# Kernel tuning notes

Hardware: AMD Instinct MI355X
Metric: run time of the kernel (lower is better)

The kernel has to match this reference:

```python
import jax, jax.numpy as jnp
import numpy as np

B, T, C = 4, 2048, 1024


def setup_inputs() -> dict:
    key = jax.random.key(0)
    ks = jax.random.split(key, 5)
    s = 1.0 / np.sqrt(C)
    return {
        "X": jax.random.normal(ks[0], (B, T, C), dtype=jnp.float32),
        "Wq": jax.random.normal(ks[1], (C, C), dtype=jnp.float32) * s,
        "Wk": jax.random.normal(ks[2], (C, C), dtype=jnp.float32) * s,
        "Wv": jax.random.normal(ks[3], (C, C), dtype=jnp.float32) * s,
        "Wo": jax.random.normal(ks[4], (C, C), dtype=jnp.float32) * s,
    }


def reference(X, Wq, Wk, Wv, Wo):
    Bx, Tx, Cx = X.shape
    Q = X @ Wq  # [B,T,C]
    K = X @ Wk
    V = X @ Wv
    scores = jnp.einsum('btc,bsc->bts', Q, K) / jnp.sqrt(jnp.asarray(Cx, X.dtype))
    # causal mask: position t attends to s <= t
    causal = jnp.tril(jnp.ones((Tx, Tx), dtype=bool))
    scores = jnp.where(causal, scores, jnp.asarray(-jnp.inf, scores.dtype))
    weights = jax.nn.softmax(scores, axis=-1)
    out = jnp.einsum('bts,bsc->btc', weights, V)
    return out @ Wo
```

## Files before the change

### kernel.cpp

```cpp
#include <hip/hip_runtime.h>
#include <hip/hip_bf16.h>
#include <cmath>


typedef __attribute__((ext_vector_type(8))) __bf16 bf16x8;
typedef __attribute__((ext_vector_type(8))) short short8;
typedef __attribute__((ext_vector_type(4))) float f32x4;

__device__ __forceinline__ unsigned short f2bf(float f) {
  union { float f; unsigned u; } v; v.f = f;
  unsigned u = v.u;
  u += ((u >> 16) & 1u) + 0x7fffu;
  return (unsigned short)(u >> 16);
}
__device__ __forceinline__ float bf2f(unsigned short h) {
  union { unsigned u; float f; } v; v.u = ((unsigned)h) << 16;
  return v.f;
}

#define GLDS(gp, sp)                                                           \
  __builtin_amdgcn_global_load_lds(                                            \
      (const __attribute__((address_space(1))) void*)(gp),                     \
      (__attribute__((address_space(3))) void*)(sp), 16, 0, 0)

__global__ void cast_kernel(const float* __restrict__ src,
                            unsigned short* __restrict__ dst, int n) {
  int i = (blockIdx.x * blockDim.x + threadIdx.x) * 4;
  if (i >= n) return;
  float4 f = *(const float4*)(src + i);
  ushort4 o = make_ushort4(f2bf(f.x), f2bf(f.y), f2bf(f.z), f2bf(f.w));
  *(ushort4*)(dst + i) = o;
}

__global__ void transpose_cast(const float* __restrict__ src,
                               unsigned short* __restrict__ dst,
                               int rows, int cols) {
  __shared__ float tile[32][33];
  int bx = blockIdx.x * 32;
  int by = blockIdx.y * 32;
  int tx = threadIdx.x;
  int ty = threadIdx.y;
#pragma unroll
  for (int i = 0; i < 32; i += 8)
    tile[ty + i][tx] = src[(size_t)(by + ty + i) * cols + bx + tx];
  __syncthreads();
#pragma unroll
  for (int i = 0; i < 32; i += 8)
    dst[(size_t)(bx + ty + i) * rows + by + tx] = f2bf(tile[tx][ty + i]);
}

template <typename OutT>
__global__ __launch_bounds__(256, 2)
void gemm_bt(const unsigned short* __restrict__ A, int lda, long long sA,
             const unsigned short* __restrict__ B, int ldb, long long sB,
             OutT* __restrict__ Cp, int ldc, long long sC,
             int K, float alpha, int tri, int kcap) {
  A  += (long long)blockIdx.z * sA;
  B  += (long long)blockIdx.z * sB;
  Cp += (long long)blockIdx.z * sC;

  int by, bx;
  if (tri) {
    const int idx = blockIdx.x;
    by = (int)((sqrtf(8.f * idx + 1.f) - 1.f) * 0.5f);
    while (by * (by + 1) / 2 > idx) --by;
    while ((by + 1) * (by + 2) / 2 <= idx) ++by;
    bx = idx - by * (by + 1) / 2;
  } else {
    by = blockIdx.y;
    bx = blockIdx.x;
  }
  const int m0 = by * 128;
  const int n0 = bx * 128;
  const int Keff = kcap ? min(K, m0 + 128) : K;

  const int tid  = threadIdx.x;
  const int lane = tid & 63;
  const int w    = tid >> 6;
  const int wm   = (w >> 1) * 64;
  const int wn   = (w & 1) * 64;
  const int quad = lane >> 4;
  const int l16  = lane & 15;

  __shared__ unsigned short As[128 * 64];
  __shared__ unsigned short Bs[128 * 64];

  f32x4 acc[4][4];
#pragma unroll
  for (int i = 0; i < 4; ++i)
#pragma unroll
    for (int j = 0; j < 4; ++j)
      acc[i][j] = (f32x4){0.f, 0.f, 0.f, 0.f};

  const int srow = tid >> 3;
  const int scol = ((tid & 7) ^ (srow & 7)) * 8;
  const unsigned short* gA = A + (long long)(m0 + srow) * lda + scol;
  const unsigned short* gB = B + (long long)(n0 + srow) * ldb + scol;
  const int rsw = l16 & 7;

  for (int kt = 0; kt < Keff; kt += 64) {
    __syncthreads();
#pragma unroll
    for (int r = 0; r < 4; ++r) {
      GLDS(gA + (long long)(r * 32) * lda + kt, As + r * 2048 + tid * 8);
      GLDS(gB + (long long)(r * 32) * ldb + kt, Bs + r * 2048 + tid * 8);
    }
    __syncthreads();
#pragma unroll
    for (int ks = 0; ks < 2; ++ks) {
      bf16x8 af[4], bfr[4];
#pragma unroll
      for (int i = 0; i < 4; ++i)
        af[i] = *(const bf16x8*)(As + (wm + i * 16 + l16) * 64 +
                                 ((ks * 4 + quad) ^ rsw) * 8);
#pragma unroll
      for (int j = 0; j < 4; ++j)
        bfr[j] = *(const bf16x8*)(Bs + (wn + j * 16 + l16) * 64 +
                                  ((ks * 4 + quad) ^ rsw) * 8);
#pragma unroll
      for (int i = 0; i < 4; ++i)
#pragma unroll
        for (int j = 0; j < 4; ++j)
          acc[i][j] = __builtin_amdgcn_mfma_f32_16x16x32_bf16(af[i], bfr[j],
                                                              acc[i][j], 0, 0, 0);
    }
  }

#pragma unroll
  for (int i = 0; i < 4; ++i) {
#pragma unroll
    for (int j = 0; j < 4; ++j) {
#pragma unroll
      for (int r = 0; r < 4; ++r) {
        const int row = m0 + wm + i * 16 + quad * 4 + r;
        const int col = n0 + wn + j * 16 + l16;
        float v = acc[i][j][r] * alpha;
        if constexpr (sizeof(OutT) == 2)
          Cp[(long long)row * ldc + col] = (OutT)f2bf(v);
        else
          Cp[(long long)row * ldc + col] = v;
      }
    }
  }
}

__global__ __launch_bounds__(256)
void softmax_causal(unsigned short* __restrict__ S, int T) {
  const long long row = blockIdx.x;
  const int t = (int)(row & (long long)(T - 1));
  const int limit = ((t >> 7) + 1) << 7;
  unsigned short* p = S + row * T;
  const int tid  = threadIdx.x;
  const int base = tid * 8;
  const bool active = base < limit;

  short8 raw = {};
  if (active) raw = *(const short8*)(p + base);
  float x[8];
  float mx = -1e30f;
#pragma unroll
  for (int j = 0; j < 8; ++j) {
    bool valid = active && (base + j) <= t;
    x[j] = valid ? bf2f((unsigned short)raw[j]) : -1e30f;
    mx = fmaxf(mx, x[j]);
  }
#pragma unroll
  for (int off = 32; off > 0; off >>= 1) mx = fmaxf(mx, __shfl_xor(mx, off));
  __shared__ float red[8];
  const int wv = tid >> 6;
  if ((tid & 63) == 0) red[wv] = mx;
  __syncthreads();
  mx = fmaxf(fmaxf(red[0], red[1]), fmaxf(red[2], red[3]));

  float sum = 0.f;
#pragma unroll
  for (int j = 0; j < 8; ++j) {
    bool valid = active && (base + j) <= t;
    x[j] = valid ? __expf(x[j] - mx) : 0.f;
    sum += x[j];
  }
#pragma unroll
  for (int off = 32; off > 0; off >>= 1) sum += __shfl_xor(sum, off);
  if ((tid & 63) == 0) red[4 + wv] = sum;
  __syncthreads();
  sum = red[4] + red[5] + red[6] + red[7];
  const float inv = 1.f / sum;

  if (active) {
    unsigned short out[8];
#pragma unroll
    for (int j = 0; j < 8; ++j) out[j] = f2bf(x[j] * inv);
    *(short8*)(p + base) = *(const short8*)out;
  }
}

extern "C" void kernel_launch(void* const* d_in, const int* in_sizes, int n_in,
                              void* d_out, int out_size, void* d_ws,
                              size_t ws_size, hipStream_t stream) {
  (void)in_sizes; (void)n_in; (void)out_size; (void)ws_size;
  const int Bb = 4, T = 2048, C = 1024;
  const int M = Bb * T;

  const float* X  = (const float*)d_in[0];
  const float* Wq = (const float*)d_in[1];
  const float* Wk = (const float*)d_in[2];
  const float* Wv = (const float*)d_in[3];
  const float* Wo = (const float*)d_in[4];
  float* Out = (float*)d_out;

  char* w = (char*)d_ws;
  unsigned short* Xb  = (unsigned short*)w; w += (size_t)M * C * 2;
  unsigned short* Wqt = (unsigned short*)w; w += (size_t)C * C * 2;
  unsigned short* Wkt = (unsigned short*)w; w += (size_t)C * C * 2;
  unsigned short* Wvt = (unsigned short*)w; w += (size_t)C * C * 2;
  unsigned short* Wot = (unsigned short*)w; w += (size_t)C * C * 2;
  unsigned short* Q   = (unsigned short*)w; w += (size_t)M * C * 2;
  unsigned short* Kb  = (unsigned short*)w; w += (size_t)M * C * 2;
  unsigned short* Vt  = (unsigned short*)w; w += (size_t)M * C * 2;
  unsigned short* O   = Xb;
  unsigned short* S   = (unsigned short*)d_out;

  cast_kernel<<<(M * C) / 4 / 256, 256, 0, stream>>>(X, Xb, M * C);
  dim3 tb(32, 8), tg(C / 32, C / 32);
  transpose_cast<<<tg, tb, 0, stream>>>(Wq, Wqt, C, C);
  transpose_cast<<<tg, tb, 0, stream>>>(Wk, Wkt, C, C);
  transpose_cast<<<tg, tb, 0, stream>>>(Wv, Wvt, C, C);
  transpose_cast<<<tg, tb, 0, stream>>>(Wo, Wot, C, C);

  dim3 blk(256);
  gemm_bt<unsigned short><<<dim3(C / 128, M / 128, 1), blk, 0, stream>>>(
      Xb, C, 0, Wqt, C, 0, Q, C, 0, C, 1.f, 0, 0);
  gemm_bt<unsigned short><<<dim3(C / 128, M / 128, 1), blk, 0, stream>>>(
      Xb, C, 0, Wkt, C, 0, Kb, C, 0, C, 1.f, 0, 0);
  gemm_bt<unsigned short><<<dim3(T / 128, C / 128, Bb), blk, 0, stream>>>(
      Wvt, C, 0, Xb, C, (long long)T * C, Vt, T, (long long)C * T, C, 1.f, 0, 0);
  const int ntri = (T / 128) * (T / 128 + 1) / 2;
  gemm_bt<unsigned short><<<dim3(ntri, 1, Bb), blk, 0, stream>>>(
      Q, C, (long long)T * C, Kb, C, (long long)T * C,
      S, T, (long long)T * T, C, 0.03125f, 1, 0);
  softmax_causal<<<M, 256, 0, stream>>>(S, T);
  gemm_bt<unsigned short><<<dim3(C / 128, T / 128, Bb), blk, 0, stream>>>(
      S, T, (long long)T * T, Vt, T, (long long)C * T,
      O, C, (long long)T * C, T, 1.f, 0, 1);
  gemm_bt<float><<<dim3(C / 128, M / 128, 1), blk, 0, stream>>>(
      O, C, 0, Wot, C, 0, Out, C, 0, C, 1.f, 0, 0);
}
```

Before: 288.8 us.

## Fuse QKV projections into one GEMM with grouped tile ordering

```diff
diff --git a/kernel.cpp b/kernel.cpp
--- a/kernel.cpp
+++ b/kernel.cpp
@@ -32,21 +32,26 @@
   *(ushort4*)(dst + i) = o;
 }
 
-__global__ void transpose_cast(const float* __restrict__ src,
-                               unsigned short* __restrict__ dst,
-                               int rows, int cols) {
+__global__ void transpose4(const float* __restrict__ w0,
+                           const float* __restrict__ w1,
+                           const float* __restrict__ w2,
+                           const float* __restrict__ w3,
+                           unsigned short* __restrict__ wcat,
+                           unsigned short* __restrict__ wot,
+                           int n) {
+  const float* src = blockIdx.z == 0 ? w0 : blockIdx.z == 1 ? w1
+                     : blockIdx.z == 2 ? w2 : w3;
+  unsigned short* dst = blockIdx.z < 3 ? wcat + (size_t)blockIdx.z * n * n : wot;
   __shared__ float tile[32][33];
-  int bx = blockIdx.x * 32;
-  int by = blockIdx.y * 32;
-  int tx = threadIdx.x;
-  int ty = threadIdx.y;
+  int bx = blockIdx.x * 32, by = blockIdx.y * 32;
+  int tx = threadIdx.x, ty = threadIdx.y;
 #pragma unroll
   for (int i = 0; i < 32; i += 8)
-    tile[ty + i][tx] = src[(size_t)(by + ty + i) * cols + bx + tx];
+    tile[ty + i][tx] = src[(size_t)(by + ty + i) * n + bx + tx];
   __syncthreads();
 #pragma unroll
   for (int i = 0; i < 32; i += 8)
-    dst[(size_t)(bx + ty + i) * rows + by + tx] = f2bf(tile[tx][ty + i]);
+    dst[(size_t)(bx + ty + i) * n + by + tx] = f2bf(tile[tx][ty + i]);
 }
 
 template <typename OutT>
@@ -54,7 +59,7 @@
 void gemm_bt(const unsigned short* __restrict__ A, int lda, long long sA,
              const unsigned short* __restrict__ B, int ldb, long long sB,
              OutT* __restrict__ Cp, int ldc, long long sC,
-             int K, float alpha, int tri, int kcap) {
+             int K, float alpha, int tri, int kcap, int gx, int qkv) {
   A  += (long long)blockIdx.z * sA;
   B  += (long long)blockIdx.z * sB;
   Cp += (long long)blockIdx.z * sC;
@@ -66,6 +71,12 @@
     while (by * (by + 1) / 2 > idx) --by;
     while ((by + 1) * (by + 2) / 2 <= idx) ++by;
     bx = idx - by * (by + 1) / 2;
+  } else if (gx > 0) {
+    const int id = blockIdx.x;
+    const int gs = gx * 8;
+    const int g = id / gs, r = id - g * gs;
+    bx = r >> 3;
+    by = g * 8 + (r & 7);
   } else {
     by = blockIdx.y;
     bx = blockIdx.x;
@@ -130,15 +141,32 @@
   for (int i = 0; i < 4; ++i) {
 #pragma unroll
     for (int j = 0; j < 4; ++j) {
-#pragma unroll
-      for (int r = 0; r < 4; ++r) {
-        const int row = m0 + wm + i * 16 + quad * 4 + r;
-        const int col = n0 + wn + j * 16 + l16;
-        float v = acc[i][j][r] * alpha;
-        if constexpr (sizeof(OutT) == 2)
-          Cp[(long long)row * ldc + col] = (OutT)f2bf(v);
-        else
-          Cp[(long long)row * ldc + col] = v;
+      const int row = m0 + wm + i * 16 + quad * 4;
+      const int col = n0 + wn + j * 16 + l16;
+      if constexpr (sizeof(OutT) == 2) {
+        if (qkv) {
+          if (col >= 2048) {
+            const int b = row >> 11, t = row & 2047, cv = col - 2048;
+            ushort4 o = make_ushort4(f2bf(acc[i][j][0]), f2bf(acc[i][j][1]),
+                                     f2bf(acc[i][j][2]), f2bf(acc[i][j][3]));
+            *(ushort4*)((unsigned short*)Cp + 16777216LL +
+                        ((long long)(b * 1024 + cv)) * 2048 + t) = o;
+          } else {
+            unsigned short* dst =
+                (unsigned short*)Cp + (col >= 1024 ? 8388608LL - 1024 : 0);
+#pragma unroll
+            for (int r = 0; r < 4; ++r)
+              dst[(long long)(row + r) * 1024 + col] = f2bf(acc[i][j][r]);
+          }
+          continue;
+        }
+#pragma unroll
+        for (int r = 0; r < 4; ++r)
+          Cp[(long long)(row + r) * ldc + col] = (OutT)f2bf(acc[i][j][r] * alpha);
+      } else {
+#pragma unroll
+        for (int r = 0; r < 4; ++r)
+          Cp[(long long)(row + r) * ldc + col] = acc[i][j][r] * alpha;
       }
     }
   }
@@ -209,39 +237,30 @@
   float* Out = (float*)d_out;
 
   char* w = (char*)d_ws;
-  unsigned short* Xb  = (unsigned short*)w; w += (size_t)M * C * 2;
-  unsigned short* Wqt = (unsigned short*)w; w += (size_t)C * C * 2;
-  unsigned short* Wkt = (unsigned short*)w; w += (size_t)C * C * 2;
-  unsigned short* Wvt = (unsigned short*)w; w += (size_t)C * C * 2;
-  unsigned short* Wot = (unsigned short*)w; w += (size_t)C * C * 2;
-  unsigned short* Q   = (unsigned short*)w; w += (size_t)M * C * 2;
-  unsigned short* Kb  = (unsigned short*)w; w += (size_t)M * C * 2;
-  unsigned short* Vt  = (unsigned short*)w; w += (size_t)M * C * 2;
-  unsigned short* O   = Xb;
-  unsigned short* S   = (unsigned short*)d_out;
+  unsigned short* Xb   = (unsigned short*)w; w += (size_t)M * C * 2;
+  unsigned short* Wcat = (unsigned short*)w; w += (size_t)3 * C * C * 2;
+  unsigned short* Wot  = (unsigned short*)w; w += (size_t)C * C * 2;
+  unsigned short* Q    = (unsigned short*)w; w += (size_t)M * C * 2;
+  unsigned short* Kb   = (unsigned short*)w; w += (size_t)M * C * 2;
+  unsigned short* Vt   = (unsigned short*)w; w += (size_t)M * C * 2;
+  unsigned short* O    = Xb;
+  unsigned short* S    = (unsigned short*)d_out;
 
   cast_kernel<<<(M * C) / 4 / 256, 256, 0, stream>>>(X, Xb, M * C);
-  dim3 tb(32, 8), tg(C / 32, C / 32);
-  transpose_cast<<<tg, tb, 0, stream>>>(Wq, Wqt, C, C);
-  transpose_cast<<<tg, tb, 0, stream>>>(Wk, Wkt, C, C);
-  transpose_cast<<<tg, tb, 0, stream>>>(Wv, Wvt, C, C);
-  transpose_cast<<<tg, tb, 0, stream>>>(Wo, Wot, C, C);
+  transpose4<<<dim3(C / 32, C / 32, 4), dim3(32, 8), 0, stream>>>(
+      Wq, Wk, Wv, Wo, Wcat, Wot, C);
 
   dim3 blk(256);
-  gemm_bt<unsigned short><<<dim3(C / 128, M / 128, 1), blk, 0, stream>>>(
-      Xb, C, 0, Wqt, C, 0, Q, C, 0, C, 1.f, 0, 0);
-  gemm_bt<unsigned short><<<dim3(C / 128, M / 128, 1), blk, 0, stream>>>(
-      Xb, C, 0, Wkt, C, 0, Kb, C, 0, C, 1.f, 0, 0);
-  gemm_bt<unsigned short><<<dim3(T / 128, C / 128, Bb), blk, 0, stream>>>(
-      Wvt, C, 0, Xb, C, (long long)T * C, Vt, T, (long long)C * T, C, 1.f, 0, 0);
+  gemm_bt<unsigned short><<<dim3((3 * C / 128) * (M / 128), 1, 1), blk, 0, stream>>>(
+      Xb, C, 0, Wcat, C, 0, Q, C, 0, C, 1.f, 0, 0, 3 * C / 128, 1);
   const int ntri = (T / 128) * (T / 128 + 1) / 2;
   gemm_bt<unsigned short><<<dim3(ntri, 1, Bb), blk, 0, stream>>>(
       Q, C, (long long)T * C, Kb, C, (long long)T * C,
-      S, T, (long long)T * T, C, 0.03125f, 1, 0);
+      S, T, (long long)T * T, C, 0.03125f, 1, 0, 0, 0);
   softmax_causal<<<M, 256, 0, stream>>>(S, T);
-  gemm_bt<unsigned short><<<dim3(C / 128, T / 128, Bb), blk, 0, stream>>>(
+  gemm_bt<unsigned short><<<dim3((C / 128) * (T / 128), 1, Bb), blk, 0, stream>>>(
       S, T, (long long)T * T, Vt, T, (long long)C * T,
-      O, C, (long long)T * C, T, 1.f, 0, 1);
-  gemm_bt<float><<<dim3(C / 128, M / 128, 1), blk, 0, stream>>>(
-      O, C, 0, Wot, C, 0, Out, C, 0, C, 1.f, 0, 0);
-}
+      O, C, (long long)T * C, T, 1.f, 0, 1, C / 128, 0);
+  gemm_bt<float><<<dim3((C / 128) * (M / 128), 1, 1), blk, 0, stream>>>(
+      O, C, 0, Wot, C, 0, Out, C, 0, C, 1.f, 0, 0, C / 128, 0);
+}
```

New measurement: 274.9 us. 1.05x faster.
